# Kernel tuning notes

Hardware: AMD Instinct MI355X
Metric: run time of the kernel (lower is better)

The kernel has to match this reference:

```python
import jax, jax.numpy as jnp
import numpy as np

NUM_NODES = 50000
IN_CH = 64
OUT_CH = 64
NUM_EDGES = 800000


def setup_inputs() -> dict:
    key = jax.random.key(0)
    k1, k2, k3, k4 = jax.random.split(key, 4)
    x = jax.random.normal(k1, (NUM_NODES, IN_CH), dtype=jnp.float32)
    edge_index = jax.random.randint(k2, (2, NUM_EDGES), 0, NUM_NODES, dtype=jnp.int64)
    # Xavier-uniform linear weight [out, 2*in], zero bias (torch convention W @ x^T + b)
    fan_in, fan_out = 2 * IN_CH, OUT_CH
    limit = np.sqrt(6.0 / (fan_in + fan_out))
    W = jax.random.uniform(k3, (OUT_CH, 2 * IN_CH), minval=-limit, maxval=limit, dtype=jnp.float32)
    b = jnp.zeros((OUT_CH,), dtype=jnp.float32)
    return {"x": x, "edge_index": edge_index, "W": W, "b": b}


def reference(x, edge_index, W, b):
    num_nodes = x.shape[0]
    row, col = edge_index[0], edge_index[1]
    # mean aggregation: scatter-add of x[row] into destination col, divide by degree
    aggr = jax.ops.segment_sum(x[row], col, num_segments=num_nodes)  # [N, C]
    deg = jax.ops.segment_sum(jnp.ones_like(col, dtype=x.dtype), col, num_segments=num_nodes)
    aggr = aggr / jnp.clip(deg, 1.0, None)[:, None]
    out = jnp.concatenate([x, aggr], axis=-1)  # [N, 2C]
    return out @ W.T + b
```

## Files before the change

kernel.cpp:

```cpp
#include <hip/hip_runtime.h>
#include <hip/hip_fp8.h>

#define NN 50000
#define NC 64
#define NE 800000
#define NGRP 3125
#define CAP 62
#define CONV_BLK 3125
#define FILL_BLK 782
#define EPB 1024
#define NPART 196
#define QCAP 4608
#define QSTRIDE 32
#define TS 288

typedef __attribute__((ext_vector_type(8))) short bf16x8;
typedef __attribute__((ext_vector_type(4))) float f32x4;
typedef __attribute__((ext_vector_type(2))) float f32x2;

__device__ __forceinline__ unsigned short f32_to_bf16_rne(float v) {
    unsigned u = __float_as_uint(v);
    u = (u + 0x7fffu + ((u >> 16) & 1u)) >> 16;
    return (unsigned short)u;
}
__device__ __forceinline__ unsigned pack_bf16x2(float lo, float hi) {
    return (unsigned)f32_to_bf16_rne(lo) | ((unsigned)f32_to_bf16_rne(hi) << 16);
}

__device__ __forceinline__ unsigned char f32_to_fp8(float v) {
    __hip_fp8_e4m3 t(v);
    return (unsigned char)t.__x;
}
__device__ __forceinline__ float fp8_to_f32(unsigned b) {
    __hip_fp8_e4m3 t;
    t.__x = (__hip_fp8_storage_t)b;
    return (float)t;
}

#if __has_builtin(__builtin_amdgcn_cvt_pk_f32_fp8)
template <bool HI>
__device__ __forceinline__ f32x2 cvtpk(unsigned u) {
    return __builtin_amdgcn_cvt_pk_f32_fp8(u, HI);
}
#else
template <bool HI>
__device__ __forceinline__ f32x2 cvtpk(unsigned u) {
    f32x2 r;
    r.x = fp8_to_f32((u >> (HI ? 16 : 0)) & 0xffu);
    r.y = fp8_to_f32((u >> (HI ? 24 : 8)) & 0xffu);
    return r;
}
#endif
__device__ __forceinline__ f32x2 pk_fma(f32x2 a, f32x2 b, f32x2 c) {
    f32x2 d;
    asm("v_pk_fma_f32 %0, %1, %2, %3" : "=v"(d) : "v"(a), "v"(b), "v"(c));
    return d;
}

__global__ __launch_bounds__(256) void convert_partition_kernel(
        const float4* __restrict__ x4, ushort4* __restrict__ xh4,
        unsigned* __restrict__ xf8,
        const int4* __restrict__ row4, const int4* __restrict__ col4,
        int* __restrict__ qcnt, unsigned* __restrict__ queue,
        const float4* __restrict__ W4, ushort4* __restrict__ wb4) {
    int b = blockIdx.x;
    if (b >= FILL_BLK + CONV_BLK) {
#pragma unroll
        for (int j = 0; j < 8; ++j) {
            int i = threadIdx.x + 256 * j;
            float4 v = W4[i];
            ushort4 h;
            h.x = f32_to_bf16_rne(v.x); h.y = f32_to_bf16_rne(v.y);
            h.z = f32_to_bf16_rne(v.z); h.w = f32_to_bf16_rne(v.w);
            wb4[i] = h;
        }
        return;
    }
    if (b >= FILL_BLK) {
        int i = (b - FILL_BLK) * 256 + threadIdx.x;
        float4 v = x4[i];
        ushort4 h;
        h.x = f32_to_bf16_rne(v.x); h.y = f32_to_bf16_rne(v.y);
        h.z = f32_to_bf16_rne(v.z); h.w = f32_to_bf16_rne(v.w);
        xh4[i] = h;
        unsigned q = (unsigned)f32_to_fp8(v.x)
                   | ((unsigned)f32_to_fp8(v.y) << 8)
                   | ((unsigned)f32_to_fp8(v.z) << 16)
                   | ((unsigned)f32_to_fp8(v.w) << 24);
        xf8[i] = q;
        return;
    }
    __shared__ int lcnt[NPART];
    __shared__ int lstart[NPART];
    __shared__ int sbase[NPART];
    __shared__ int wpart[4];
    __shared__ int stot;
    __shared__ unsigned staged[EPB];

    const int tid = threadIdx.x;
    for (int i = tid; i < NPART; i += 256) lcnt[i] = 0;
    __syncthreads();

    unsigned ent[4];
    int      rk[4];
    int t = b * 256 + tid;
    const int nv = (t < NE / 4);
    if (nv) {
        int4 r = row4[t];
        int4 c = col4[t];
        int p;
        p = c.x >> 8; ent[0] = ((unsigned)p << 24) | ((unsigned)(c.x & 255) << 16) | (unsigned)r.x;
        rk[0] = atomicAdd(&lcnt[p], 1);
        p = c.y >> 8; ent[1] = ((unsigned)p << 24) | ((unsigned)(c.y & 255) << 16) | (unsigned)r.y;
        rk[1] = atomicAdd(&lcnt[p], 1);
        p = c.z >> 8; ent[2] = ((unsigned)p << 24) | ((unsigned)(c.z & 255) << 16) | (unsigned)r.z;
        rk[2] = atomicAdd(&lcnt[p], 1);
        p = c.w >> 8; ent[3] = ((unsigned)p << 24) | ((unsigned)(c.w & 255) << 16) | (unsigned)r.w;
        rk[3] = atomicAdd(&lcnt[p], 1);
    }
    __syncthreads();

    int v = (tid < NPART) ? lcnt[tid] : 0;
    int sc = v;
    const int lane2 = tid & 63;
#pragma unroll
    for (int d = 1; d < 64; d <<= 1) {
        int u = __shfl_up(sc, (unsigned)d, 64);
        if (lane2 >= d) sc += u;
    }
    if (lane2 == 63) wpart[tid >> 6] = sc;
    __syncthreads();
    {
        int wid2 = tid >> 6;
        int add = 0;
        if (wid2 > 0) add += wpart[0];
        if (wid2 > 1) add += wpart[1];
        if (wid2 > 2) add += wpart[2];
        int incl = sc + add;
        if (tid < NPART) {
            lstart[tid] = incl - v;
            sbase[tid]  = atomicAdd(&qcnt[tid * QSTRIDE], v);
        }
        if (tid == 255) stot = incl;
    }
    __syncthreads();

    if (nv) {
#pragma unroll
        for (int k = 0; k < 4; ++k) {
            unsigned e = ent[k];
            staged[lstart[e >> 24] + rk[k]] = e;
        }
    }
    __syncthreads();

    int tot = stot;
    for (int i = tid; i < tot; i += 256) {
        unsigned e = staged[i];
        int p = (int)(e >> 24);
        int pos = sbase[p] + (i - lstart[p]);
        if (pos < QCAP) queue[p * QCAP + pos] = e;
    }
}

__global__ __launch_bounds__(512) void build_records_kernel(
        const int* __restrict__ qcnt, const unsigned* __restrict__ queue,
        uint4* __restrict__ rec4) {
    __shared__ __align__(16) unsigned short lslot[256 * 66];
    __shared__ int lcnt[256];
    const int p = blockIdx.x;
    const int tid = threadIdx.x;
    if (tid < 256) lcnt[tid] = 0;
    __syncthreads();

    int qn = min(qcnt[p * QSTRIDE], QCAP);
    const unsigned* q = queue + p * QCAP;
    for (int i = tid; i < qn; i += 512) {
        unsigned e = q[i];
        int n = (int)((e >> 16) & 255u);
        int pos = atomicAdd(&lcnt[n], 1);
        if (pos < CAP)
            lslot[n * 66 + pos] = (unsigned short)(e & 0xffffu);
    }
    __syncthreads();

    const unsigned* ls = (const unsigned*)lslot;
    uint4* dst = rec4 + (size_t)p * 2048;
#pragma unroll
    for (int it = 0; it < 4; ++it) {
        int i = tid + 512 * it;
        int n = i >> 3, c = i & 7;
        int base = n * 33 + 4 * c - 1;
        uint4 g;
        if (c == 0) {
            g.x = (unsigned)lcnt[n];
            g.y = ls[n * 33 + 0];
            g.z = ls[n * 33 + 1];
            g.w = ls[n * 33 + 2];
        } else {
            g.x = ls[base];
            g.y = ls[base + 1];
            g.z = ls[base + 2];
            g.w = ls[base + 3];
        }
        dst[i] = g;
    }
}

__global__ __launch_bounds__(256) void gather_mfma_kernel(
        const uint4* __restrict__ xq,
        const uint2* __restrict__ xf,
        const int*   __restrict__ rec,
        const uint4* __restrict__ Wq,
        const float* __restrict__ b,
        float*       __restrict__ out) {
    __shared__ __align__(16) char tile[16 * TS];

    const int lane = threadIdx.x & 63;
    const int w    = threadIdx.x >> 6;
    const int g8   = lane >> 3;
    const int c8   = lane & 7;
    const int mg   = lane >> 4;
    const int mc   = lane & 15;

    const unsigned short* slots = (const unsigned short*)rec;

    {
        const int gi   = blockIdx.x;
        const int base = gi * 16;
        const int n0   = base + w * 4;

        int d0 = rec[(n0 + 0) << 5], d1 = rec[(n0 + 1) << 5],
            d2 = rec[(n0 + 2) << 5], d3 = rec[(n0 + 3) << 5];
        int l0 = min(d0, CAP), l1 = min(d1, CAP), l2 = min(d2, CAP), l3 = min(d3, CAP);
        int m  = max(max(l0, l1), max(l2, l3));
        int itn = (m + 7) >> 3;
        const int k0 = ((n0 + 0) << 6) + 2, k1 = ((n0 + 1) << 6) + 2,
                  k2 = ((n0 + 2) << 6) + 2, k3 = ((n0 + 3) << 6) + 2;

        f32x2 G0[4], G1[4], G2[4], G3[4];
#pragma unroll
        for (int j = 0; j < 4; ++j) {
            G0[j] = (f32x2)0.f; G1[j] = (f32x2)0.f;
            G2[j] = (f32x2)0.f; G3[j] = (f32x2)0.f;
        }
#define ACC8F8(G, wk, u) { \
        f32x2 p0 = cvtpk<false>(u.x), p1 = cvtpk<true>(u.x); \
        f32x2 p2 = cvtpk<false>(u.y), p3 = cvtpk<true>(u.y); \
        G[0] = pk_fma(wk, p0, G[0]); G[1] = pk_fma(wk, p1, G[1]); \
        G[2] = pk_fma(wk, p2, G[2]); G[3] = pk_fma(wk, p3, G[3]); }
        for (int it = 0, e = g8; it < itn; it += 2, e += 16) {
            int eb = e + 8;
            int a0 = (int)slots[k0 + e],  a1 = (int)slots[k1 + e],
                a2 = (int)slots[k2 + e],  a3 = (int)slots[k3 + e];
            int b0 = (int)slots[k0 + eb], b1 = (int)slots[k1 + eb],
                b2 = (int)slots[k2 + eb], b3 = (int)slots[k3 + eb];
            int sa0 = (e  < l0) ? a0 : 0;  float ma0 = (e  < l0) ? 1.f : 0.f;
            int sa1 = (e  < l1) ? a1 : 0;  float ma1 = (e  < l1) ? 1.f : 0.f;
            int sa2 = (e  < l2) ? a2 : 0;  float ma2 = (e  < l2) ? 1.f : 0.f;
            int sa3 = (e  < l3) ? a3 : 0;  float ma3 = (e  < l3) ? 1.f : 0.f;
            int sb0 = (eb < l0) ? b0 : 0;  float mb0 = (eb < l0) ? 1.f : 0.f;
            int sb1 = (eb < l1) ? b1 : 0;  float mb1 = (eb < l1) ? 1.f : 0.f;
            int sb2 = (eb < l2) ? b2 : 0;  float mb2 = (eb < l2) ? 1.f : 0.f;
            int sb3 = (eb < l3) ? b3 : 0;  float mb3 = (eb < l3) ? 1.f : 0.f;
            uint2 ua0 = xf[sa0 * 8 + c8];
            uint2 ua1 = xf[sa1 * 8 + c8];
            uint2 ua2 = xf[sa2 * 8 + c8];
            uint2 ua3 = xf[sa3 * 8 + c8];
            uint2 ub0 = xf[sb0 * 8 + c8];
            uint2 ub1 = xf[sb1 * 8 + c8];
            uint2 ub2 = xf[sb2 * 8 + c8];
            uint2 ub3 = xf[sb3 * 8 + c8];
            f32x2 wa0; wa0.x = ma0; wa0.y = ma0;
            f32x2 wa1; wa1.x = ma1; wa1.y = ma1;
            f32x2 wa2; wa2.x = ma2; wa2.y = ma2;
            f32x2 wa3; wa3.x = ma3; wa3.y = ma3;
            f32x2 wb0; wb0.x = mb0; wb0.y = mb0;
            f32x2 wb1; wb1.x = mb1; wb1.y = mb1;
            f32x2 wb2; wb2.x = mb2; wb2.y = mb2;
            f32x2 wb3; wb3.x = mb3; wb3.y = mb3;
            ACC8F8(G0, wa0, ua0) ACC8F8(G0, wb0, ub0)
            ACC8F8(G1, wa1, ua1) ACC8F8(G1, wb1, ub1)
            ACC8F8(G2, wa2, ua2) ACC8F8(G2, wb2, ub2)
            ACC8F8(G3, wa3, ua3) ACC8F8(G3, wb3, ub3)
        }
#undef ACC8F8

        bf16x8 bfrag[4];
        {
            const uint4* wr = Wq + ((16 * w + mc) * 16 + mg);
#pragma unroll
            for (int ks = 0; ks < 4; ++ks)
                bfrag[ks] = *(const bf16x8*)(wr + ks * 4);
        }
        const float bv = b[16 * w + mc];

#define RED8(G) \
        _Pragma("unroll") \
        for (int j = 0; j < 4; ++j) { \
            G[j].x += __shfl_xor(G[j].x, 8, 64); \
            G[j].x += __shfl_xor(G[j].x, 16, 64); \
            G[j].x += __shfl_xor(G[j].x, 32, 64); \
            G[j].y += __shfl_xor(G[j].y, 8, 64); \
            G[j].y += __shfl_xor(G[j].y, 16, 64); \
            G[j].y += __shfl_xor(G[j].y, 32, 64); \
        }
        RED8(G0) RED8(G1) RED8(G2) RED8(G3)
#undef RED8

        float inv0 = 1.0f / fmaxf((float)d0, 1.0f);
        float inv1 = 1.0f / fmaxf((float)d1, 1.0f);
        float inv2 = 1.0f / fmaxf((float)d2, 1.0f);
        float inv3 = 1.0f / fmaxf((float)d3, 1.0f);

        if (lane < 32) {
            int nk = lane >> 3, ch = lane & 7;
            uint4 sv = xq[(n0 + nk) * 8 + ch];
            *(uint4*)(tile + (w * 4 + nk) * TS + ch * 16) = sv;
        }
        if (lane < 8) {
            uint4 mv;
            mv.x = pack_bf16x2(G0[0].x * inv0, G0[0].y * inv0);
            mv.y = pack_bf16x2(G0[1].x * inv0, G0[1].y * inv0);
            mv.z = pack_bf16x2(G0[2].x * inv0, G0[2].y * inv0);
            mv.w = pack_bf16x2(G0[3].x * inv0, G0[3].y * inv0);
            *(uint4*)(tile + (w * 4 + 0) * TS + 128 + lane * 16) = mv;
            mv.x = pack_bf16x2(G1[0].x * inv1, G1[0].y * inv1);
            mv.y = pack_bf16x2(G1[1].x * inv1, G1[1].y * inv1);
            mv.z = pack_bf16x2(G1[2].x * inv1, G1[2].y * inv1);
            mv.w = pack_bf16x2(G1[3].x * inv1, G1[3].y * inv1);
            *(uint4*)(tile + (w * 4 + 1) * TS + 128 + lane * 16) = mv;
            mv.x = pack_bf16x2(G2[0].x * inv2, G2[0].y * inv2);
            mv.y = pack_bf16x2(G2[1].x * inv2, G2[1].y * inv2);
            mv.z = pack_bf16x2(G2[2].x * inv2, G2[2].y * inv2);
            mv.w = pack_bf16x2(G2[3].x * inv2, G2[3].y * inv2);
            *(uint4*)(tile + (w * 4 + 2) * TS + 128 + lane * 16) = mv;
            mv.x = pack_bf16x2(G3[0].x * inv3, G3[0].y * inv3);
            mv.y = pack_bf16x2(G3[1].x * inv3, G3[1].y * inv3);
            mv.z = pack_bf16x2(G3[2].x * inv3, G3[2].y * inv3);
            mv.w = pack_bf16x2(G3[3].x * inv3, G3[3].y * inv3);
            *(uint4*)(tile + (w * 4 + 3) * TS + 128 + lane * 16) = mv;
        }
        __syncthreads();

        f32x4 acc = {bv, bv, bv, bv};
#pragma unroll
        for (int ks = 0; ks < 4; ++ks) {
            bf16x8 af = *(const bf16x8*)(tile + mc * TS + ks * 64 + mg * 16);
            acc = __builtin_amdgcn_mfma_f32_16x16x32_bf16(af, bfrag[ks], acc, 0, 0, 0);
        }

#pragma unroll
        for (int r = 0; r < 4; ++r)
            out[(base + mg * 4 + r) * NC + 16 * w + mc] = acc[r];
    }
}

extern "C" void kernel_launch(void* const* d_in, const int* in_sizes, int n_in,
                              void* d_out, int out_size, void* d_ws, size_t ws_size,
                              hipStream_t stream) {
    const float* x   = (const float*)d_in[0];
    const int*   ei  = (const int*)d_in[1];
    const float* W   = (const float*)d_in[2];
    const float* b   = (const float*)d_in[3];
    float*       out = (float*)d_out;

    const int* row = ei;
    const int* col = ei + NE;

    int*      qcnt  = (int*)d_ws;
    unsigned* queue = (unsigned*)(qcnt + NPART * QSTRIDE);
    int*      rec   = (int*)(queue + (size_t)NPART * QCAP);
    unsigned short* xh = (unsigned short*)(rec + (size_t)50176 * 32);
    unsigned* xf8 = (unsigned*)(xh + (size_t)NN * NC);
    unsigned short* wb = (unsigned short*)(xf8 + (size_t)NN * NC / 4);

    (void)hipMemsetAsync(qcnt, 0, NPART * QSTRIDE * sizeof(int), stream);

    convert_partition_kernel<<<FILL_BLK + CONV_BLK + 1, 256, 0, stream>>>(
        (const float4*)x, (ushort4*)xh, xf8, (const int4*)row, (const int4*)col,
        qcnt, queue, (const float4*)W, (ushort4*)wb);

    build_records_kernel<<<NPART, 512, 0, stream>>>(
        qcnt, queue, (uint4*)rec);

    gather_mfma_kernel<<<NGRP, 256, 0, stream>>>(
        (const uint4*)xh, (const uint2*)xf8, rec, (const uint4*)wb, b, out);
}
```

Measured before the change: 116.1 us.

## Fuse record building into gather-MFMA kernel using shared-memory slot lists

Removes the separate build_records kernel and its global rec buffer. Each fused block handles 64 destination nodes: it scans its partition's queue, keeps only entries for its quarter, builds per-node slot lists in LDS, then runs the gather and MFMA over four 16-node groups. This drops one launch and a global write/read round trip. In exchange each partition queue is read four times, grid size falls from 3125 to 782 blocks, and per-block work becomes serial across groups with extra barriers.

```diff
diff --git a/kernel.cpp b/kernel.cpp
--- a/kernel.cpp
+++ b/kernel.cpp
@@ -4,7 +4,6 @@
 #define NN 50000
 #define NC 64
 #define NE 800000
-#define NGRP 3125
 #define CAP 62
 #define CONV_BLK 3125
 #define FILL_BLK 782
@@ -13,6 +12,7 @@
 #define QCAP 4608
 #define QSTRIDE 32
 #define TS 288
+#define FUSE_BLK 782
 
 typedef __attribute__((ext_vector_type(8))) short bf16x8;
 typedef __attribute__((ext_vector_type(4))) float f32x4;
@@ -163,86 +163,76 @@
     }
 }
 
-__global__ __launch_bounds__(512) void build_records_kernel(
-        const int* __restrict__ qcnt, const unsigned* __restrict__ queue,
-        uint4* __restrict__ rec4) {
-    __shared__ __align__(16) unsigned short lslot[256 * 66];
-    __shared__ int lcnt[256];
-    const int p = blockIdx.x;
-    const int tid = threadIdx.x;
-    if (tid < 256) lcnt[tid] = 0;
-    __syncthreads();
-
-    int qn = min(qcnt[p * QSTRIDE], QCAP);
-    const unsigned* q = queue + p * QCAP;
-    for (int i = tid; i < qn; i += 512) {
-        unsigned e = q[i];
-        int n = (int)((e >> 16) & 255u);
-        int pos = atomicAdd(&lcnt[n], 1);
-        if (pos < CAP)
-            lslot[n * 66 + pos] = (unsigned short)(e & 0xffffu);
-    }
-    __syncthreads();
-
-    const unsigned* ls = (const unsigned*)lslot;
-    uint4* dst = rec4 + (size_t)p * 2048;
-#pragma unroll
-    for (int it = 0; it < 4; ++it) {
-        int i = tid + 512 * it;
-        int n = i >> 3, c = i & 7;
-        int base = n * 33 + 4 * c - 1;
-        uint4 g;
-        if (c == 0) {
-            g.x = (unsigned)lcnt[n];
-            g.y = ls[n * 33 + 0];
-            g.z = ls[n * 33 + 1];
-            g.w = ls[n * 33 + 2];
-        } else {
-            g.x = ls[base];
-            g.y = ls[base + 1];
-            g.z = ls[base + 2];
-            g.w = ls[base + 3];
-        }
-        dst[i] = g;
-    }
-}
-
-__global__ __launch_bounds__(256) void gather_mfma_kernel(
+__global__ __launch_bounds__(256) void build_gather_mfma_kernel(
+        const int*   __restrict__ qcnt, const unsigned* __restrict__ queue,
         const uint4* __restrict__ xq,
         const uint2* __restrict__ xf,
-        const int*   __restrict__ rec,
         const uint4* __restrict__ Wq,
         const float* __restrict__ b,
         float*       __restrict__ out) {
+    __shared__ unsigned short lslot[64 * 66];
+    __shared__ int lcnt[64];
     __shared__ __align__(16) char tile[16 * TS];
 
-    const int lane = threadIdx.x & 63;
-    const int w    = threadIdx.x >> 6;
+    const int j   = blockIdx.x;
+    const int nb  = j * 64;
+    if (nb >= NN) return;
+    const int p   = j >> 2;
+    const int sub = j & 3;
+    const int tid = threadIdx.x;
+
+    if (tid < 64) lcnt[tid] = 0;
+    __syncthreads();
+
+    int qn = min(qcnt[p * QSTRIDE], QCAP);
+    const unsigned* q = queue + p * QCAP;
+    for (int i = tid; i < qn; i += 256) {
+        unsigned e = q[i];
+        int d8 = (int)((e >> 16) & 255u);
+        if ((d8 >> 6) == sub) {
+            int n = d8 & 63;
+            int pos = atomicAdd(&lcnt[n], 1);
+            if (pos < CAP)
+                lslot[n * 66 + pos] = (unsigned short)(e & 0xffffu);
+        }
+    }
+    __syncthreads();
+
+    const int lane = tid & 63;
+    const int w    = tid >> 6;
     const int g8   = lane >> 3;
     const int c8   = lane & 7;
     const int mg   = lane >> 4;
     const int mc   = lane & 15;
 
-    const unsigned short* slots = (const unsigned short*)rec;
-
+    bf16x8 bfrag[4];
     {
-        const int gi   = blockIdx.x;
-        const int base = gi * 16;
-        const int n0   = base + w * 4;
-
-        int d0 = rec[(n0 + 0) << 5], d1 = rec[(n0 + 1) << 5],
-            d2 = rec[(n0 + 2) << 5], d3 = rec[(n0 + 3) << 5];
-        int l0 = min(d0, CAP), l1 = min(d1, CAP), l2 = min(d2, CAP), l3 = min(d3, CAP);
+        const uint4* wr = Wq + ((16 * w + mc) * 16 + mg);
+#pragma unroll
+        for (int ks = 0; ks < 4; ++ks)
+            bfrag[ks] = *(const bf16x8*)(wr + ks * 4);
+    }
+    const float bv = b[16 * w + mc];
+
+    for (int g = 0; g < 4; ++g) {
+        const int base = nb + g * 16;
+        if (base >= NN) break;
+        const int n0l = g * 16 + w * 4;
+
+        int d0 = lcnt[n0l + 0], d1 = lcnt[n0l + 1],
+            d2 = lcnt[n0l + 2], d3 = lcnt[n0l + 3];
+        int l0 = min(d0, CAP), l1 = min(d1, CAP),
+            l2 = min(d2, CAP), l3 = min(d3, CAP);
         int m  = max(max(l0, l1), max(l2, l3));
         int itn = (m + 7) >> 3;
-        const int k0 = ((n0 + 0) << 6) + 2, k1 = ((n0 + 1) << 6) + 2,
-                  k2 = ((n0 + 2) << 6) + 2, k3 = ((n0 + 3) << 6) + 2;
+        const int k0 = (n0l + 0) * 66, k1 = (n0l + 1) * 66,
+                  k2 = (n0l + 2) * 66, k3 = (n0l + 3) * 66;
 
         f32x2 G0[4], G1[4], G2[4], G3[4];
 #pragma unroll
-        for (int j = 0; j < 4; ++j) {
-            G0[j] = (f32x2)0.f; G1[j] = (f32x2)0.f;
-            G2[j] = (f32x2)0.f; G3[j] = (f32x2)0.f;
+        for (int jj = 0; jj < 4; ++jj) {
+            G0[jj] = (f32x2)0.f; G1[jj] = (f32x2)0.f;
+            G2[jj] = (f32x2)0.f; G3[jj] = (f32x2)0.f;
         }
 #define ACC8F8(G, wk, u) { \
         f32x2 p0 = cvtpk<false>(u.x), p1 = cvtpk<true>(u.x); \
@@ -251,10 +241,10 @@
         G[2] = pk_fma(wk, p2, G[2]); G[3] = pk_fma(wk, p3, G[3]); }
         for (int it = 0, e = g8; it < itn; it += 2, e += 16) {
             int eb = e + 8;
-            int a0 = (int)slots[k0 + e],  a1 = (int)slots[k1 + e],
-                a2 = (int)slots[k2 + e],  a3 = (int)slots[k3 + e];
-            int b0 = (int)slots[k0 + eb], b1 = (int)slots[k1 + eb],
-                b2 = (int)slots[k2 + eb], b3 = (int)slots[k3 + eb];
+            int a0 = (int)lslot[k0 + e],  a1 = (int)lslot[k1 + e],
+                a2 = (int)lslot[k2 + e],  a3 = (int)lslot[k3 + e];
+            int b0 = (int)lslot[k0 + eb], b1 = (int)lslot[k1 + eb],
+                b2 = (int)lslot[k2 + eb], b3 = (int)lslot[k3 + eb];
             int sa0 = (e  < l0) ? a0 : 0;  float ma0 = (e  < l0) ? 1.f : 0.f;
             int sa1 = (e  < l1) ? a1 : 0;  float ma1 = (e  < l1) ? 1.f : 0.f;
             int sa2 = (e  < l2) ? a2 : 0;  float ma2 = (e  < l2) ? 1.f : 0.f;
@@ -286,24 +276,15 @@
         }
 #undef ACC8F8
 
-        bf16x8 bfrag[4];
-        {
-            const uint4* wr = Wq + ((16 * w + mc) * 16 + mg);
-#pragma unroll
-            for (int ks = 0; ks < 4; ++ks)
-                bfrag[ks] = *(const bf16x8*)(wr + ks * 4);
-        }
-        const float bv = b[16 * w + mc];
-
 #define RED8(G) \
         _Pragma("unroll") \
-        for (int j = 0; j < 4; ++j) { \
-            G[j].x += __shfl_xor(G[j].x, 8, 64); \
-            G[j].x += __shfl_xor(G[j].x, 16, 64); \
-            G[j].x += __shfl_xor(G[j].x, 32, 64); \
-            G[j].y += __shfl_xor(G[j].y, 8, 64); \
-            G[j].y += __shfl_xor(G[j].y, 16, 64); \
-            G[j].y += __shfl_xor(G[j].y, 32, 64); \
+        for (int jj = 0; jj < 4; ++jj) { \
+            G[jj].x += __shfl_xor(G[jj].x, 8, 64); \
+            G[jj].x += __shfl_xor(G[jj].x, 16, 64); \
+            G[jj].x += __shfl_xor(G[jj].x, 32, 64); \
+            G[jj].y += __shfl_xor(G[jj].y, 8, 64); \
+            G[jj].y += __shfl_xor(G[jj].y, 16, 64); \
+            G[jj].y += __shfl_xor(G[jj].y, 32, 64); \
         }
         RED8(G0) RED8(G1) RED8(G2) RED8(G3)
 #undef RED8
@@ -315,7 +296,7 @@
 
         if (lane < 32) {
             int nk = lane >> 3, ch = lane & 7;
-            uint4 sv = xq[(n0 + nk) * 8 + ch];
+            uint4 sv = xq[(base + w * 4 + nk) * 8 + ch];
             *(uint4*)(tile + (w * 4 + nk) * TS + ch * 16) = sv;
         }
         if (lane < 8) {
@@ -353,6 +334,8 @@
 #pragma unroll
         for (int r = 0; r < 4; ++r)
             out[(base + mg * 4 + r) * NC + 16 * w + mc] = acc[r];
+
+        __syncthreads();
     }
 }
 
@@ -370,8 +353,7 @@
 
     int*      qcnt  = (int*)d_ws;
     unsigned* queue = (unsigned*)(qcnt + NPART * QSTRIDE);
-    int*      rec   = (int*)(queue + (size_t)NPART * QCAP);
-    unsigned short* xh = (unsigned short*)(rec + (size_t)50176 * 32);
+    unsigned short* xh = (unsigned short*)(queue + (size_t)NPART * QCAP);
     unsigned* xf8 = (unsigned*)(xh + (size_t)NN * NC);
     unsigned short* wb = (unsigned short*)(xf8 + (size_t)NN * NC / 4);
 
@@ -381,9 +363,7 @@
         (const float4*)x, (ushort4*)xh, xf8, (const int4*)row, (const int4*)col,
         qcnt, queue, (const float4*)W, (ushort4*)wb);
 
-    build_records_kernel<<<NPART, 512, 0, stream>>>(
-        qcnt, queue, (uint4*)rec);
-
-    gather_mfma_kernel<<<NGRP, 256, 0, stream>>>(
-        (const uint4*)xh, (const uint2*)xf8, rec, (const uint4*)wb, b, out);
-}
+    build_gather_mfma_kernel<<<FUSE_BLK, 256, 0, stream>>>(
+        qcnt, queue, (const uint4*)xh, (const uint2*)xf8,
+        (const uint4*)wb, b, out);
+}
```

After: 124.0 us. 6.8% more time.
